# Kernel tuning notes

Hardware: AMD Instinct MI355X
Metric: run time of the kernel (lower is better)

Reference implementation:

```python
import jax, jax.numpy as jnp
import numpy as np


def setup_inputs() -> dict:
    key = jax.random.key(0)
    k1, k2, k3 = jax.random.split(key, 3)
    B, K, OUT, IN = 8192, 8, 1024, 1024
    bound = (6.0 / (IN * OUT)) ** 0.5
    x = jax.random.normal(k1, (B, IN), dtype=jnp.float32)
    expert_weights = jax.random.uniform(k2, (B, K), dtype=jnp.float32)
    weight = jax.random.uniform(k3, (K, OUT, IN), dtype=jnp.float32, minval=-bound, maxval=bound)
    bias = jnp.zeros((K, OUT), dtype=jnp.float32)
    return {"x": x, "expert_weights": expert_weights, "weight": weight, "bias": bias}


def reference(x, expert_weights, weight, bias):
    # Mathematically identical to: blended_W = einsum('bk,koi->boi'); bmm(blended_W, x)
    # but avoids materializing the [B,out,in] intermediate: apply each expert's
    # linear map then blend with routing weights (contraction reassociation).
    per_expert = jnp.einsum('bi,koi->bko', x, weight)        # [B, K, out]
    y = jnp.einsum('bk,bko->bo', expert_weights, per_expert)  # [B, out]
    y = y + expert_weights @ bias                             # blended bias [B, out]
    return y
```

## Files before the change

### kernel.cpp

```cpp
#include <hip/hip_runtime.h>
#include <hip/hip_bf16.h>

typedef __attribute__((ext_vector_type(8))) short short8;
typedef __attribute__((ext_vector_type(4))) float f32x4;

#define NDIM 1024
#define INDIM 1024
#define KEXP 8
#define BROWS 8192
#define NX (BROWS * INDIM)
#define NW (KEXP * NDIM * INDIM)

#define BM 256
#define BN 128
#define BK 64
#define NT 128
#define ABUF 16384
#define BBUF 8192
#define BUFU (ABUF + BBUF)

__device__ __forceinline__ unsigned int pack2bf(float a, float b) {
    __hip_bfloat162 h = __float22bfloat162_rn(make_float2(a, b));
    union { __hip_bfloat162 h; unsigned int u; } cv;
    cv.h = h;
    return cv.u;
}

__device__ __forceinline__ void gload16(const void* src, void* ldsdst) {
    __builtin_amdgcn_global_load_lds(
        (__attribute__((address_space(1))) void*)(src),
        (__attribute__((address_space(3))) void*)(ldsdst), 16, 0, 0);
}

__global__ void convert_bf16(const float* __restrict__ x, const float* __restrict__ w,
                             unsigned short* __restrict__ dst) {
    const long total = (long)NX + NW;
    const long stride = (long)gridDim.x * blockDim.x * 8;
    for (long i = ((long)blockIdx.x * blockDim.x + threadIdx.x) * 8; i < total; i += stride) {
        const float* s = (i < NX) ? (x + i) : (w + (i - NX));
        float4 a = ((const float4*)s)[0];
        float4 b = ((const float4*)s)[1];
        uint4 q;
        q.x = pack2bf(a.x, a.y); q.y = pack2bf(a.z, a.w);
        q.z = pack2bf(b.x, b.y); q.w = pack2bf(b.z, b.w);
        *(uint4*)(dst + i) = q;
    }
}

__global__ __launch_bounds__(512, 2)
void moe_gemm_pipe(const unsigned short* __restrict__ ab,
                   const float* __restrict__ ew,
                   const float* __restrict__ bias,
                   float* __restrict__ out) {
    __shared__ __align__(16) unsigned short lds[3 * BUFU];

    const int tid = threadIdx.x;
    const int bid = blockIdx.x;
    const int nt = bid & 7;
    const int mt = bid >> 3;
    const int mbase = mt * BM;
    const int nbase = nt * BN;

    const int w  = tid >> 6;
    const int l  = tid & 63;
    const int lr = l & 15;
    const int lg = l >> 4;
    const int wrow = (w >> 1) * 64;
    const int wcol = (w & 1) * 64;

    const int lrow = l >> 2;
    const int sg = (l & 3) ^ ((l >> 3) & 3);

    const unsigned short* Xb = ab;
    const unsigned short* Wb = ab + NX;

    const int swz = (lr >> 1) & 3;
    int aoff[4][2], boff[4][2];
#pragma unroll
    for (int m = 0; m < 4; ++m)
#pragma unroll
        for (int ks = 0; ks < 2; ++ks)
            aoff[m][ks] = ks * 8192 + (wrow + m * 16 + lr) * 32 + ((lg ^ swz) * 8);
#pragma unroll
    for (int n = 0; n < 4; ++n)
#pragma unroll
        for (int ks = 0; ks < 2; ++ks)
            boff[n][ks] = ABUF + ks * 4096 + (wcol + n * 16 + lr) * 32 + ((lg ^ swz) * 8);

    auto stageA = [&](int buf, int kt, int i) {
        const int c = i * 8 + w;
        const int ks = c >> 4, rg = c & 15;
        const unsigned short* src = Xb + (size_t)(mbase + rg * 16 + lrow) * INDIM
                                  + (size_t)((kt & 15) * 64 + ks * 32 + sg * 8);
        gload16(src, &lds[buf * BUFU + c * 512]);
    };
    auto stageB = [&](int buf, int kt, int i) {
        const int c = i * 8 + w;
        const int ks = c >> 3, rg = c & 7;
        const unsigned short* src = Wb + (size_t)(kt >> 4) * (NDIM * INDIM)
                                  + (size_t)(nbase + rg * 16 + lrow) * INDIM
                                  + (size_t)((kt & 15) * 64 + ks * 32 + sg * 8);
        gload16(src, &lds[buf * BUFU + ABUF + c * 512]);
    };

    f32x4 acc[4][4], accT[4][4];
#pragma unroll
    for (int m = 0; m < 4; ++m)
#pragma unroll
        for (int n = 0; n < 4; ++n) {
            acc[m][n] = f32x4{0.f, 0.f, 0.f, 0.f};
            accT[m][n] = f32x4{0.f, 0.f, 0.f, 0.f};
        }

#pragma unroll
    for (int t = 0; t < 2; ++t) {
        stageA(t, t, 0); stageA(t, t, 1); stageA(t, t, 2); stageA(t, t, 3);
        stageB(t, t, 0); stageB(t, t, 1);
    }

    int bufR = 0, bufS = 2;
#pragma unroll 1
    for (int kt = 0; kt < NT; ++kt) {
        const bool doS = (kt + 2) < NT;
        const bool bnd = (kt & 15) == 15;

        if (kt < NT - 2)
            asm volatile("s_waitcnt vmcnt(6)\n\ts_barrier" ::: "memory");
        else
            asm volatile("s_waitcnt vmcnt(0)\n\ts_barrier" ::: "memory");

        float e0[4][4];
        if (bnd) {
            const int eidx = kt >> 4;
#pragma unroll
            for (int m = 0; m < 4; ++m)
#pragma unroll
                for (int j = 0; j < 4; ++j)
                    e0[m][j] = ew[(size_t)(mbase + wrow + m * 16 + lg * 4 + j) * KEXP + eidx];
        }

        const unsigned short* lb = &lds[bufR * BUFU];
        short8 a0[4], b0[4], a1[4], b1[4];

#pragma unroll
        for (int m = 0; m < 4; ++m) a0[m] = *(const short8*)(lb + aoff[m][0]);
#pragma unroll
        for (int n = 0; n < 4; ++n) b0[n] = *(const short8*)(lb + boff[n][0]);

        if (doS) {
            stageA(bufS, kt + 2, 0); stageA(bufS, kt + 2, 1);
            stageA(bufS, kt + 2, 2); stageA(bufS, kt + 2, 3);
            stageB(bufS, kt + 2, 0); stageB(bufS, kt + 2, 1);
        }

#pragma unroll
        for (int m = 0; m < 4; ++m) a1[m] = *(const short8*)(lb + aoff[m][1]);
#pragma unroll
        for (int n = 0; n < 4; ++n) b1[n] = *(const short8*)(lb + boff[n][1]);

        __builtin_amdgcn_s_setprio(1);
#pragma unroll
        for (int m = 0; m < 4; ++m)
#pragma unroll
            for (int n = 0; n < 4; ++n)
                acc[m][n] = __builtin_amdgcn_mfma_f32_16x16x32_bf16(a0[m], b0[n], acc[m][n], 0, 0, 0);
        __builtin_amdgcn_s_setprio(0);

        __builtin_amdgcn_s_setprio(1);
#pragma unroll
        for (int m = 0; m < 4; ++m)
#pragma unroll
            for (int n = 0; n < 4; ++n)
                acc[m][n] = __builtin_amdgcn_mfma_f32_16x16x32_bf16(a1[m], b1[n], acc[m][n], 0, 0, 0);
        __builtin_amdgcn_s_setprio(0);

        if (bnd) {
#pragma unroll
            for (int m = 0; m < 4; ++m)
#pragma unroll
                for (int n = 0; n < 4; ++n) {
#pragma unroll
                    for (int j = 0; j < 4; ++j)
                        accT[m][n][j] += e0[m][j] * acc[m][n][j];
                    acc[m][n] = f32x4{0.f, 0.f, 0.f, 0.f};
                }
        }

        bufR = (bufR == 2) ? 0 : bufR + 1;
        bufS = (bufS == 2) ? 0 : bufS + 1;
    }

    float bv[4][8];
#pragma unroll
    for (int n = 0; n < 4; ++n) {
        const int gc = nbase + wcol + n * 16 + lr;
#pragma unroll
        for (int kk = 0; kk < 8; ++kk) bv[n][kk] = bias[kk * NDIM + gc];
    }
#pragma unroll
    for (int m = 0; m < 4; ++m)
#pragma unroll
        for (int j = 0; j < 4; ++j) {
            const int grow = mbase + wrow + m * 16 + lg * 4 + j;
            const float4* e4 = (const float4*)(ew + (size_t)grow * KEXP);
            const float4 ea = e4[0];
            const float4 eb = e4[1];
            const float ev[8] = {ea.x, ea.y, ea.z, ea.w, eb.x, eb.y, eb.z, eb.w};
            float* op = out + (size_t)grow * NDIM + nbase + wcol;
#pragma unroll
            for (int n = 0; n < 4; ++n) {
                float t = accT[m][n][j];
#pragma unroll
                for (int kk = 0; kk < 8; ++kk) t += ev[kk] * bv[n][kk];
                op[n * 16 + lr] = t;
            }
        }
}

#define FLDW 40
__global__ __launch_bounds__(256, 2)
void moe_blend_gemm_fb(const float* __restrict__ x, const float* __restrict__ ew,
                       const float* __restrict__ w, const float* __restrict__ bias,
                       float* __restrict__ out) {
    __shared__ unsigned short lA[128][FLDW];
    __shared__ unsigned short lB[128][FLDW];
    const int tid = threadIdx.x, bid = blockIdx.x;
    const int nt = bid & 7, mt = bid >> 3;
    const int mbase = mt * 128, nbase = nt * 128;
    const int trow = tid >> 1, tcol = (tid & 1) * 16;
    const float* xp = x + (size_t)(mbase + trow) * INDIM + tcol;
    const float* wp = w + (size_t)(nbase + trow) * INDIM + tcol;
    const float* ep = ew + (size_t)(mbase + trow) * KEXP;
    const int wid = tid >> 6, wrB = (wid >> 1) * 64, wcB = (wid & 1) * 64;
    const int l = tid & 63, lr = l & 15, lg = l >> 4;
    f32x4 acc[4][4];
#pragma unroll
    for (int m = 0; m < 4; ++m)
#pragma unroll
        for (int n = 0; n < 4; ++n) acc[m][n] = f32x4{0.f, 0.f, 0.f, 0.f};
    const unsigned short* rdA = &lA[wrB + lr][lg * 8];
    const unsigned short* rdB = &lB[wcB + lr][lg * 8];
    unsigned int* wA = (unsigned int*)&lA[trow][tcol];
    unsigned int* wB = (unsigned int*)&lB[trow][tcol];
    float4 ra0, ra1, ra2, ra3, rb0, rb1, rb2, rb3;
    float sc;
    {
        const float4* pa = (const float4*)(xp);
        ra0 = pa[0]; ra1 = pa[1]; ra2 = pa[2]; ra3 = pa[3];
        const float4* pb = (const float4*)(wp);
        rb0 = pb[0]; rb1 = pb[1]; rb2 = pb[2]; rb3 = pb[3];
        sc = ep[0];
    }
    for (int tt = 0; tt < 256; ++tt) {
        __syncthreads();
        uint4 qa0, qa1, qb0, qb1;
        qa0.x = pack2bf(ra0.x * sc, ra0.y * sc); qa0.y = pack2bf(ra0.z * sc, ra0.w * sc);
        qa0.z = pack2bf(ra1.x * sc, ra1.y * sc); qa0.w = pack2bf(ra1.z * sc, ra1.w * sc);
        qa1.x = pack2bf(ra2.x * sc, ra2.y * sc); qa1.y = pack2bf(ra2.z * sc, ra2.w * sc);
        qa1.z = pack2bf(ra3.x * sc, ra3.y * sc); qa1.w = pack2bf(ra3.z * sc, ra3.w * sc);
        qb0.x = pack2bf(rb0.x, rb0.y); qb0.y = pack2bf(rb0.z, rb0.w);
        qb0.z = pack2bf(rb1.x, rb1.y); qb0.w = pack2bf(rb1.z, rb1.w);
        qb1.x = pack2bf(rb2.x, rb2.y); qb1.y = pack2bf(rb2.z, rb2.w);
        qb1.z = pack2bf(rb3.x, rb3.y); qb1.w = pack2bf(rb3.z, rb3.w);
        *(uint4*)(wA) = qa0; *(uint4*)(wA + 4) = qa1;
        *(uint4*)(wB) = qb0; *(uint4*)(wB + 4) = qb1;
        __syncthreads();
        if (tt + 1 < 256) {
            const int kc = (tt + 1) >> 5, i0 = ((tt + 1) & 31) * 32;
            const float4* pa = (const float4*)(xp + i0);
            ra0 = pa[0]; ra1 = pa[1]; ra2 = pa[2]; ra3 = pa[3];
            const float4* pb = (const float4*)(wp + (size_t)kc * (size_t)(NDIM * INDIM) + i0);
            rb0 = pb[0]; rb1 = pb[1]; rb2 = pb[2]; rb3 = pb[3];
            sc = ep[kc];
        }
        short8 af[4], bf[4];
#pragma unroll
        for (int m = 0; m < 4; ++m) af[m] = *(const short8*)(rdA + m * 16 * FLDW);
#pragma unroll
        for (int n = 0; n < 4; ++n) bf[n] = *(const short8*)(rdB + n * 16 * FLDW);
#pragma unroll
        for (int m = 0; m < 4; ++m)
#pragma unroll
            for (int n = 0; n < 4; ++n)
                acc[m][n] = __builtin_amdgcn_mfma_f32_16x16x32_bf16(af[m], bf[n], acc[m][n], 0, 0, 0);
    }
#pragma unroll
    for (int m = 0; m < 4; ++m)
#pragma unroll
        for (int j = 0; j < 4; ++j) {
            const int gr = mbase + wrB + m * 16 + lg * 4 + j;
            const float4* e4 = (const float4*)(ew + (size_t)gr * KEXP);
            const float4 e0 = e4[0], e1 = e4[1];
            const float eb[8] = {e0.x, e0.y, e0.z, e0.w, e1.x, e1.y, e1.z, e1.w};
            float* op = out + (size_t)gr * NDIM + nbase + wcB;
#pragma unroll
            for (int n = 0; n < 4; ++n) {
                float t = acc[m][n][j];
#pragma unroll
                for (int kk = 0; kk < 8; ++kk) t += eb[kk] * bias[kk * NDIM + nbase + wcB + n * 16 + lr];
                op[n * 16 + lr] = t;
            }
        }
}

extern "C" void kernel_launch(void* const* d_in, const int* in_sizes, int n_in,
                              void* d_out, int out_size, void* d_ws, size_t ws_size,
                              hipStream_t stream) {
    (void)in_sizes; (void)n_in; (void)out_size;
    const float* x    = (const float*)d_in[0];
    const float* ew   = (const float*)d_in[1];
    const float* w    = (const float*)d_in[2];
    const float* bias = (const float*)d_in[3];
    float* out = (float*)d_out;

    const size_t need = (size_t)(NX + NW) * sizeof(unsigned short);
    if (ws_size >= need) {
        unsigned short* ab = (unsigned short*)d_ws;
        hipLaunchKernelGGL(convert_bf16, dim3(2048), dim3(256), 0, stream, x, w, ab);
        hipLaunchKernelGGL(moe_gemm_pipe, dim3(256), dim3(512), 0, stream, ab, ew, bias, out);
    } else {
        hipLaunchKernelGGL(moe_blend_gemm_fb, dim3(512), dim3(256), 0, stream, x, ew, w, bias, out);
    }
}
```

Before: 180.1 us.

## Fold routing weights into expanded A and split-K GEMM with bf16 partials

Adds a new path that builds a pre-scaled activation matrix A'[b, k*IN+i] = ew[b,k]*x[b,i] in bf16, so the whole op becomes a single GEMM over K*IN. The GEMM uses 256x256 tiles and a two-way split along the reduction, writing bf16 partials that a separate reduce kernel sums and then adds the blended bias to. This removes the per-k-tile accumulator rescaling and the ew loads from the inner loop. In exchange it materialises a 128 MB A' buffer, rounds partials to bf16, and adds extra launches. The old fallback kernel is removed, so no path runs when the workspace is too small.

New measurement: 167.8 us. 1.07x faster.

```diff
diff --git a/kernel.cpp b/kernel.cpp
--- a/kernel.cpp
+++ b/kernel.cpp
@@ -10,6 +10,227 @@
 #define BROWS 8192
 #define NX (BROWS * INDIM)
 #define NW (KEXP * NDIM * INDIM)
+#define NA (BROWS * KEXP * INDIM)
+#define NPH (BROWS * NDIM)
+
+__device__ __forceinline__ unsigned int pack2bf(float a, float b) {
+    __hip_bfloat162 h = __float22bfloat162_rn(make_float2(a, b));
+    union { __hip_bfloat162 h; unsigned int u; } cv;
+    cv.h = h;
+    return cv.u;
+}
+
+__device__ __forceinline__ float bf2f(unsigned short u) {
+    return __uint_as_float(((unsigned int)u) << 16);
+}
+
+__device__ __forceinline__ void gload16(const void* src, void* ldsdst) {
+    __builtin_amdgcn_global_load_lds(
+        (__attribute__((address_space(1))) void*)(src),
+        (__attribute__((address_space(3))) void*)(ldsdst), 16, 0, 0);
+}
+
+
+__global__ void convert_a(const float* __restrict__ x, const float* __restrict__ ew,
+                          unsigned short* __restrict__ Ap) {
+    const int t = blockIdx.x * blockDim.x + threadIdx.x;
+    if (t >= (BROWS * INDIM / 8)) return;
+    const int b = t >> 7;
+    const int i0 = (t & 127) * 8;
+    const float4 xa = *(const float4*)(x + (size_t)b * INDIM + i0);
+    const float4 xb = *(const float4*)(x + (size_t)b * INDIM + i0 + 4);
+    const float4 ea = *(const float4*)(ew + (size_t)b * KEXP);
+    const float4 e2 = *(const float4*)(ew + (size_t)b * KEXP + 4);
+    const float e[8] = {ea.x, ea.y, ea.z, ea.w, e2.x, e2.y, e2.z, e2.w};
+    unsigned short* dst = Ap + (size_t)b * (KEXP * INDIM) + i0;
+#pragma unroll
+    for (int k = 0; k < 8; ++k) {
+        const float s = e[k];
+        uint4 q;
+        q.x = pack2bf(xa.x * s, xa.y * s);
+        q.y = pack2bf(xa.z * s, xa.w * s);
+        q.z = pack2bf(xb.x * s, xb.y * s);
+        q.w = pack2bf(xb.z * s, xb.w * s);
+        *(uint4*)(dst + (size_t)k * INDIM) = q;
+    }
+}
+
+__global__ void convert_w(const float* __restrict__ w, unsigned short* __restrict__ Wp) {
+    const long i = ((long)blockIdx.x * blockDim.x + threadIdx.x) * 8;
+    if (i >= NW) return;
+    const float4 a = ((const float4*)(w + i))[0];
+    const float4 b = ((const float4*)(w + i))[1];
+    uint4 q;
+    q.x = pack2bf(a.x, a.y); q.y = pack2bf(a.z, a.w);
+    q.z = pack2bf(b.x, b.y); q.w = pack2bf(b.z, b.w);
+    *(uint4*)(Wp + i) = q;
+}
+
+__global__ __launch_bounds__(512, 2)
+void moe_gemm_ks(const unsigned short* __restrict__ Ap,
+                 const unsigned short* __restrict__ Wp,
+                 unsigned short* __restrict__ Pp) {
+    __shared__ __align__(16) unsigned short lds[2 * 32768];
+
+    const int tid = threadIdx.x;
+    const int bid = blockIdx.x;
+    const int comp = bid & 7;
+    const int nt = comp >> 1;
+    const int h  = comp & 1;
+    const int mt = bid >> 3;
+    const int mbase = mt * 256;
+    const int nbase = nt * 256;
+    const int kofs = h * 4096;
+
+    const int w  = tid >> 6;
+    const int l  = tid & 63;
+    const int lr = l & 15;
+    const int lg = l >> 4;
+    const int wrow = (w >> 2) * 128;
+    const int wcol = (w & 3) * 64;
+
+    const int lrow = l >> 2;
+    const int sg = (l & 3) ^ ((l >> 3) & 3);
+    const int swz = (lr >> 1) & 3;
+
+    int aoff[8][2], boff[4][2];
+#pragma unroll
+    for (int mf = 0; mf < 8; ++mf)
+#pragma unroll
+        for (int ks = 0; ks < 2; ++ks)
+            aoff[mf][ks] = ks * 8192 + (wrow + mf * 16 + lr) * 32 + ((lg ^ swz) * 8);
+#pragma unroll
+    for (int nf = 0; nf < 4; ++nf)
+#pragma unroll
+        for (int ks = 0; ks < 2; ++ks)
+            boff[nf][ks] = 16384 + ks * 8192 + (wcol + nf * 16 + lr) * 32 + ((lg ^ swz) * 8);
+
+    auto stage4 = [&](int slot, int kt, int half) {
+#pragma unroll
+        for (int i = 0; i < 4; ++i) {
+            const int id = w * 8 + half * 4 + i;
+            unsigned short* dst = &lds[slot * 32768 + id * 512];
+            const int ks = (id >> 4) & 1;
+            const int sub = id & 15;
+            const int kcb = kofs + kt * 64 + ks * 32 + sg * 8;
+            if (id < 32) {
+                gload16(Ap + (size_t)(mbase + sub * 16 + lrow) * (KEXP * INDIM) + kcb, dst);
+            } else {
+                gload16(Wp + (size_t)(kcb >> 10) * (NDIM * INDIM)
+                           + (size_t)(nbase + sub * 16 + lrow) * INDIM + (kcb & 1023), dst);
+            }
+        }
+    };
+
+    f32x4 acc[8][4];
+#pragma unroll
+    for (int mf = 0; mf < 8; ++mf)
+#pragma unroll
+        for (int nf = 0; nf < 4; ++nf) acc[mf][nf] = f32x4{0.f, 0.f, 0.f, 0.f};
+
+    stage4(0, 0, 0);
+    stage4(0, 0, 1);
+
+#pragma unroll 1
+    for (int kt = 0; kt < 64; ++kt) {
+        const int cs = kt & 1;
+        const bool doS = (kt + 1) < 64;
+
+        asm volatile("s_waitcnt vmcnt(0)\n\ts_barrier" ::: "memory");
+
+        const unsigned short* lb = &lds[cs * 32768];
+        short8 alo[4], ahi[4], b0[4], b1[4];
+
+#pragma unroll
+        for (int m = 0; m < 4; ++m) alo[m] = *(const short8*)(lb + aoff[m][0]);
+#pragma unroll
+        for (int n = 0; n < 4; ++n) b0[n] = *(const short8*)(lb + boff[n][0]);
+        if (doS) stage4(cs ^ 1, kt + 1, 0);
+#pragma unroll
+        for (int m = 0; m < 4; ++m) ahi[m] = *(const short8*)(lb + aoff[4 + m][0]);
+
+        __builtin_amdgcn_s_setprio(1);
+#pragma unroll
+        for (int m = 0; m < 4; ++m)
+#pragma unroll
+            for (int n = 0; n < 4; ++n)
+                acc[m][n] = __builtin_amdgcn_mfma_f32_16x16x32_bf16(alo[m], b0[n], acc[m][n], 0, 0, 0);
+        __builtin_amdgcn_s_setprio(0);
+
+#pragma unroll
+        for (int n = 0; n < 4; ++n) b1[n] = *(const short8*)(lb + boff[n][1]);
+#pragma unroll
+        for (int m = 0; m < 4; ++m) alo[m] = *(const short8*)(lb + aoff[m][1]);
+        if (doS) stage4(cs ^ 1, kt + 1, 1);
+
+        __builtin_amdgcn_s_setprio(1);
+#pragma unroll
+        for (int m = 0; m < 4; ++m)
+#pragma unroll
+            for (int n = 0; n < 4; ++n)
+                acc[4 + m][n] = __builtin_amdgcn_mfma_f32_16x16x32_bf16(ahi[m], b0[n], acc[4 + m][n], 0, 0, 0);
+        __builtin_amdgcn_s_setprio(0);
+
+#pragma unroll
+        for (int m = 0; m < 4; ++m) ahi[m] = *(const short8*)(lb + aoff[4 + m][1]);
+
+        __builtin_amdgcn_s_setprio(1);
+#pragma unroll
+        for (int m = 0; m < 4; ++m)
+#pragma unroll
+            for (int n = 0; n < 4; ++n)
+                acc[m][n] = __builtin_amdgcn_mfma_f32_16x16x32_bf16(alo[m], b1[n], acc[m][n], 0, 0, 0);
+        __builtin_amdgcn_s_setprio(0);
+
+        __builtin_amdgcn_s_setprio(1);
+#pragma unroll
+        for (int m = 0; m < 4; ++m)
+#pragma unroll
+            for (int n = 0; n < 4; ++n)
+                acc[4 + m][n] = __builtin_amdgcn_mfma_f32_16x16x32_bf16(ahi[m], b1[n], acc[4 + m][n], 0, 0, 0);
+        __builtin_amdgcn_s_setprio(0);
+    }
+
+#pragma unroll
+    for (int mf = 0; mf < 8; ++mf)
+#pragma unroll
+        for (int j = 0; j < 4; ++j) {
+            const int grow = mbase + wrow + mf * 16 + lg * 4 + j;
+            unsigned short* op = Pp + (size_t)h * NPH + (size_t)grow * NDIM + nbase + wcol;
+#pragma unroll
+            for (int nf = 0; nf < 4; ++nf) {
+                union { __hip_bfloat16 hh; unsigned short u; } cv;
+                cv.hh = __float2bfloat16(acc[mf][nf][j]);
+                op[nf * 16 + lr] = cv.u;
+            }
+        }
+}
+
+__global__ void reduce_blend(const unsigned short* __restrict__ Pp,
+                             const float* __restrict__ ew,
+                             const float* __restrict__ bias,
+                             float* __restrict__ out) {
+    const long base = ((long)blockIdx.x * blockDim.x + threadIdx.x) * 8;
+    if (base >= NPH) return;
+    const int b = (int)(base >> 10);
+    const int o = (int)(base & 1023);
+    const short8 p0 = *(const short8*)(Pp + base);
+    const short8 p1 = *(const short8*)(Pp + NPH + base);
+    const float4 ea = *(const float4*)(ew + (size_t)b * KEXP);
+    const float4 e2 = *(const float4*)(ew + (size_t)b * KEXP + 4);
+    const float e[8] = {ea.x, ea.y, ea.z, ea.w, e2.x, e2.y, e2.z, e2.w};
+    float r[8];
+#pragma unroll
+    for (int j = 0; j < 8; ++j)
+        r[j] = bf2f((unsigned short)p0[j]) + bf2f((unsigned short)p1[j]);
+#pragma unroll
+    for (int k = 0; k < 8; ++k)
+#pragma unroll
+        for (int j = 0; j < 8; ++j) r[j] += e[k] * bias[k * NDIM + o + j];
+    *(float4*)(out + base) = make_float4(r[0], r[1], r[2], r[3]);
+    *(float4*)(out + base + 4) = make_float4(r[4], r[5], r[6], r[7]);
+}
+
 
 #define BM 256
 #define BN 128
@@ -18,19 +239,6 @@
 #define ABUF 16384
 #define BBUF 8192
 #define BUFU (ABUF + BBUF)
-
-__device__ __forceinline__ unsigned int pack2bf(float a, float b) {
-    __hip_bfloat162 h = __float22bfloat162_rn(make_float2(a, b));
-    union { __hip_bfloat162 h; unsigned int u; } cv;
-    cv.h = h;
-    return cv.u;
-}
-
-__device__ __forceinline__ void gload16(const void* src, void* ldsdst) {
-    __builtin_amdgcn_global_load_lds(
-        (__attribute__((address_space(1))) void*)(src),
-        (__attribute__((address_space(3))) void*)(ldsdst), 16, 0, 0);
-}
 
 __global__ void convert_bf16(const float* __restrict__ x, const float* __restrict__ w,
                              unsigned short* __restrict__ dst) {
@@ -141,18 +349,15 @@
 
         const unsigned short* lb = &lds[bufR * BUFU];
         short8 a0[4], b0[4], a1[4], b1[4];
-
 #pragma unroll
         for (int m = 0; m < 4; ++m) a0[m] = *(const short8*)(lb + aoff[m][0]);
 #pragma unroll
         for (int n = 0; n < 4; ++n) b0[n] = *(const short8*)(lb + boff[n][0]);
-
         if (doS) {
             stageA(bufS, kt + 2, 0); stageA(bufS, kt + 2, 1);
             stageA(bufS, kt + 2, 2); stageA(bufS, kt + 2, 3);
             stageB(bufS, kt + 2, 0); stageB(bufS, kt + 2, 1);
         }
-
 #pragma unroll
         for (int m = 0; m < 4; ++m) a1[m] = *(const short8*)(lb + aoff[m][1]);
 #pragma unroll
@@ -165,7 +370,6 @@
             for (int n = 0; n < 4; ++n)
                 acc[m][n] = __builtin_amdgcn_mfma_f32_16x16x32_bf16(a0[m], b0[n], acc[m][n], 0, 0, 0);
         __builtin_amdgcn_s_setprio(0);
-
         __builtin_amdgcn_s_setprio(1);
 #pragma unroll
         for (int m = 0; m < 4; ++m)
@@ -212,92 +416,6 @@
                 float t = accT[m][n][j];
 #pragma unroll
                 for (int kk = 0; kk < 8; ++kk) t += ev[kk] * bv[n][kk];
-                op[n * 16 + lr] = t;
-            }
-        }
-}
-
-#define FLDW 40
-__global__ __launch_bounds__(256, 2)
-void moe_blend_gemm_fb(const float* __restrict__ x, const float* __restrict__ ew,
-                       const float* __restrict__ w, const float* __restrict__ bias,
-                       float* __restrict__ out) {
-    __shared__ unsigned short lA[128][FLDW];
-    __shared__ unsigned short lB[128][FLDW];
-    const int tid = threadIdx.x, bid = blockIdx.x;
-    const int nt = bid & 7, mt = bid >> 3;
-    const int mbase = mt * 128, nbase = nt * 128;
-    const int trow = tid >> 1, tcol = (tid & 1) * 16;
-    const float* xp = x + (size_t)(mbase + trow) * INDIM + tcol;
-    const float* wp = w + (size_t)(nbase + trow) * INDIM + tcol;
-    const float* ep = ew + (size_t)(mbase + trow) * KEXP;
-    const int wid = tid >> 6, wrB = (wid >> 1) * 64, wcB = (wid & 1) * 64;
-    const int l = tid & 63, lr = l & 15, lg = l >> 4;
-    f32x4 acc[4][4];
-#pragma unroll
-    for (int m = 0; m < 4; ++m)
-#pragma unroll
-        for (int n = 0; n < 4; ++n) acc[m][n] = f32x4{0.f, 0.f, 0.f, 0.f};
-    const unsigned short* rdA = &lA[wrB + lr][lg * 8];
-    const unsigned short* rdB = &lB[wcB + lr][lg * 8];
-    unsigned int* wA = (unsigned int*)&lA[trow][tcol];
-    unsigned int* wB = (unsigned int*)&lB[trow][tcol];
-    float4 ra0, ra1, ra2, ra3, rb0, rb1, rb2, rb3;
-    float sc;
-    {
-        const float4* pa = (const float4*)(xp);
-        ra0 = pa[0]; ra1 = pa[1]; ra2 = pa[2]; ra3 = pa[3];
-        const float4* pb = (const float4*)(wp);
-        rb0 = pb[0]; rb1 = pb[1]; rb2 = pb[2]; rb3 = pb[3];
-        sc = ep[0];
-    }
-    for (int tt = 0; tt < 256; ++tt) {
-        __syncthreads();
-        uint4 qa0, qa1, qb0, qb1;
-        qa0.x = pack2bf(ra0.x * sc, ra0.y * sc); qa0.y = pack2bf(ra0.z * sc, ra0.w * sc);
-        qa0.z = pack2bf(ra1.x * sc, ra1.y * sc); qa0.w = pack2bf(ra1.z * sc, ra1.w * sc);
-        qa1.x = pack2bf(ra2.x * sc, ra2.y * sc); qa1.y = pack2bf(ra2.z * sc, ra2.w * sc);
-        qa1.z = pack2bf(ra3.x * sc, ra3.y * sc); qa1.w = pack2bf(ra3.z * sc, ra3.w * sc);
-        qb0.x = pack2bf(rb0.x, rb0.y); qb0.y = pack2bf(rb0.z, rb0.w);
-        qb0.z = pack2bf(rb1.x, rb1.y); qb0.w = pack2bf(rb1.z, rb1.w);
-        qb1.x = pack2bf(rb2.x, rb2.y); qb1.y = pack2bf(rb2.z, rb2.w);
-        qb1.z = pack2bf(rb3.x, rb3.y); qb1.w = pack2bf(rb3.z, rb3.w);
-        *(uint4*)(wA) = qa0; *(uint4*)(wA + 4) = qa1;
-        *(uint4*)(wB) = qb0; *(uint4*)(wB + 4) = qb1;
-        __syncthreads();
-        if (tt + 1 < 256) {
-            const int kc = (tt + 1) >> 5, i0 = ((tt + 1) & 31) * 32;
-            const float4* pa = (const float4*)(xp + i0);
-            ra0 = pa[0]; ra1 = pa[1]; ra2 = pa[2]; ra3 = pa[3];
-            const float4* pb = (const float4*)(wp + (size_t)kc * (size_t)(NDIM * INDIM) + i0);
-            rb0 = pb[0]; rb1 = pb[1]; rb2 = pb[2]; rb3 = pb[3];
-            sc = ep[kc];
-        }
-        short8 af[4], bf[4];
-#pragma unroll
-        for (int m = 0; m < 4; ++m) af[m] = *(const short8*)(rdA + m * 16 * FLDW);
-#pragma unroll
-        for (int n = 0; n < 4; ++n) bf[n] = *(const short8*)(rdB + n * 16 * FLDW);
-#pragma unroll
-        for (int m = 0; m < 4; ++m)
-#pragma unroll
-            for (int n = 0; n < 4; ++n)
-                acc[m][n] = __builtin_amdgcn_mfma_f32_16x16x32_bf16(af[m], bf[n], acc[m][n], 0, 0, 0);
-    }
-#pragma unroll
-    for (int m = 0; m < 4; ++m)
-#pragma unroll
-        for (int j = 0; j < 4; ++j) {
-            const int gr = mbase + wrB + m * 16 + lg * 4 + j;
-            const float4* e4 = (const float4*)(ew + (size_t)gr * KEXP);
-            const float4 e0 = e4[0], e1 = e4[1];
-            const float eb[8] = {e0.x, e0.y, e0.z, e0.w, e1.x, e1.y, e1.z, e1.w};
-            float* op = out + (size_t)gr * NDIM + nbase + wcB;
-#pragma unroll
-            for (int n = 0; n < 4; ++n) {
-                float t = acc[m][n][j];
-#pragma unroll
-                for (int kk = 0; kk < 8; ++kk) t += eb[kk] * bias[kk * NDIM + nbase + wcB + n * 16 + lr];
                 op[n * 16 + lr] = t;
             }
         }
@@ -313,12 +431,20 @@
     const float* bias = (const float*)d_in[3];
     float* out = (float*)d_out;
 
-    const size_t need = (size_t)(NX + NW) * sizeof(unsigned short);
-    if (ws_size >= need) {
+    const size_t needA = ((size_t)NA + NW + 2 * (size_t)NPH) * sizeof(unsigned short);
+    const size_t needB = (size_t)(NX + NW) * sizeof(unsigned short);
+
+    if (ws_size >= needA) {
+        unsigned short* Ap = (unsigned short*)d_ws;
+        unsigned short* Wp = Ap + NA;
+        unsigned short* Pp = Wp + NW;
+        hipLaunchKernelGGL(convert_a, dim3(4096), dim3(256), 0, stream, x, ew, Ap);
+        hipLaunchKernelGGL(convert_w, dim3(4096), dim3(256), 0, stream, w, Wp);
+        hipLaunchKernelGGL(moe_gemm_ks, dim3(256), dim3(512), 0, stream, Ap, Wp, Pp);
+        hipLaunchKernelGGL(reduce_blend, dim3(4096), dim3(256), 0, stream, Pp, ew, bias, out);
+    } else if (ws_size >= needB) {
         unsigned short* ab = (unsigned short*)d_ws;
         hipLaunchKernelGGL(convert_bf16, dim3(2048), dim3(256), 0, stream, x, w, ab);
         hipLaunchKernelGGL(moe_gemm_pipe, dim3(256), dim3(512), 0, stream, ab, ew, bias, out);
-    } else {
-        hipLaunchKernelGGL(moe_blend_gemm_fb, dim3(512), dim3(256), 0, stream, x, ew, w, bias, out);
-    }
-}
+    }
+}
```

## Fold experts into GEMM N dimension and blend in epilogue via LDS

Applied to the files above, without the earlier changes.

Restructures the GEMM so each block computes a 256-row by 32-output tile across all 8 experts at once, treating the K*OUT dimension as N. The reduction shrinks to the 1024-wide input, and the expert blend moves to the epilogue, where shuffles and an LDS buffer replace the per-expert accumulate step. The grid becomes 1024 blocks with an XCD-aware tile mapping, and the pipeline changes from triple to double buffering with a full vmcnt(0) wait each step. The conversion kernel grid is also doubled. In exchange, the x tile is reused across eight experts, but the full wait before each barrier may expose load latency.

Measured after the change: 145.9 us (median of 3 runs). -19.0%, faster.

```diff
diff --git a/kernel.cpp b/kernel.cpp
--- a/kernel.cpp
+++ b/kernel.cpp
@@ -10,14 +10,6 @@
 #define BROWS 8192
 #define NX (BROWS * INDIM)
 #define NW (KEXP * NDIM * INDIM)
-
-#define BM 256
-#define BN 128
-#define BK 64
-#define NT 128
-#define ABUF 16384
-#define BBUF 8192
-#define BUFU (ABUF + BBUF)
 
 __device__ __forceinline__ unsigned int pack2bf(float a, float b) {
     __hip_bfloat162 h = __float22bfloat162_rn(make_float2(a, b));
@@ -48,173 +40,175 @@
 }
 
 __global__ __launch_bounds__(512, 2)
-void moe_gemm_pipe(const unsigned short* __restrict__ ab,
+void moe_gemm_fold(const unsigned short* __restrict__ xb,
                    const float* __restrict__ ew,
+                   const unsigned short* __restrict__ Wp,
                    const float* __restrict__ bias,
                    float* __restrict__ out) {
-    __shared__ __align__(16) unsigned short lds[3 * BUFU];
+    __shared__ __align__(16) unsigned short lds[2 * 32768];
 
     const int tid = threadIdx.x;
     const int bid = blockIdx.x;
-    const int nt = bid & 7;
-    const int mt = bid >> 3;
-    const int mbase = mt * BM;
-    const int nbase = nt * BN;
+    const int xcd = bid & 7;
+    const int grp = bid >> 3;
+    const int bt = xcd * 4 + (grp & 3);
+    const int ot = grp >> 2;
+    const int bbase = bt * 256;
+    const int o_blk = ot * 32;
 
     const int w  = tid >> 6;
     const int l  = tid & 63;
     const int lr = l & 15;
     const int lg = l >> 4;
-    const int wrow = (w >> 1) * 64;
-    const int wcol = (w & 1) * 64;
+    const int wrow = (w >> 2) * 128;
+    const int wcol = (w & 3) * 64;
 
     const int lrow = l >> 2;
     const int sg = (l & 3) ^ ((l >> 3) & 3);
-
-    const unsigned short* Xb = ab;
-    const unsigned short* Wb = ab + NX;
-
     const int swz = (lr >> 1) & 3;
-    int aoff[4][2], boff[4][2];
-#pragma unroll
-    for (int m = 0; m < 4; ++m)
+
+    int aoff[8][2], boff[4][2];
+#pragma unroll
+    for (int mf = 0; mf < 8; ++mf)
 #pragma unroll
         for (int ks = 0; ks < 2; ++ks)
-            aoff[m][ks] = ks * 8192 + (wrow + m * 16 + lr) * 32 + ((lg ^ swz) * 8);
-#pragma unroll
-    for (int n = 0; n < 4; ++n)
+            aoff[mf][ks] = ks * 8192 + (wrow + mf * 16 + lr) * 32 + ((lg ^ swz) * 8);
+#pragma unroll
+    for (int nf = 0; nf < 4; ++nf)
 #pragma unroll
         for (int ks = 0; ks < 2; ++ks)
-            boff[n][ks] = ABUF + ks * 4096 + (wcol + n * 16 + lr) * 32 + ((lg ^ swz) * 8);
-
-    auto stageA = [&](int buf, int kt, int i) {
-        const int c = i * 8 + w;
-        const int ks = c >> 4, rg = c & 15;
-        const unsigned short* src = Xb + (size_t)(mbase + rg * 16 + lrow) * INDIM
-                                  + (size_t)((kt & 15) * 64 + ks * 32 + sg * 8);
-        gload16(src, &lds[buf * BUFU + c * 512]);
+            boff[nf][ks] = 16384 + ks * 8192 + (wcol + nf * 16 + lr) * 32 + ((lg ^ swz) * 8);
+
+    auto stage4 = [&](int slot, int kt, int half) {
+#pragma unroll
+        for (int i = 0; i < 4; ++i) {
+            const int id = w * 8 + half * 4 + i;
+            unsigned short* dst = &lds[slot * 32768 + id * 512];
+            const int sub = id & 15;
+            const int col = kt * 64 + ((id >> 4) & 1) * 32 + sg * 8;
+            if (id < 32) {
+                gload16(Wp + (size_t)(lrow & 7) * (NDIM * INDIM)
+                           + (size_t)(o_blk + sub * 2 + (lrow >> 3)) * INDIM + col, dst);
+            } else {
+                gload16(xb + (size_t)(bbase + sub * 16 + lrow) * INDIM + col, dst);
+            }
+        }
     };
-    auto stageB = [&](int buf, int kt, int i) {
-        const int c = i * 8 + w;
-        const int ks = c >> 3, rg = c & 7;
-        const unsigned short* src = Wb + (size_t)(kt >> 4) * (NDIM * INDIM)
-                                  + (size_t)(nbase + rg * 16 + lrow) * INDIM
-                                  + (size_t)((kt & 15) * 64 + ks * 32 + sg * 8);
-        gload16(src, &lds[buf * BUFU + ABUF + c * 512]);
-    };
-
-    f32x4 acc[4][4], accT[4][4];
-#pragma unroll
-    for (int m = 0; m < 4; ++m)
-#pragma unroll
-        for (int n = 0; n < 4; ++n) {
-            acc[m][n] = f32x4{0.f, 0.f, 0.f, 0.f};
-            accT[m][n] = f32x4{0.f, 0.f, 0.f, 0.f};
-        }
-
-#pragma unroll
-    for (int t = 0; t < 2; ++t) {
-        stageA(t, t, 0); stageA(t, t, 1); stageA(t, t, 2); stageA(t, t, 3);
-        stageB(t, t, 0); stageB(t, t, 1);
-    }
-
-    int bufR = 0, bufS = 2;
+
+    f32x4 acc[8][4];
+#pragma unroll
+    for (int mf = 0; mf < 8; ++mf)
+#pragma unroll
+        for (int nf = 0; nf < 4; ++nf) acc[mf][nf] = f32x4{0.f, 0.f, 0.f, 0.f};
+
+    stage4(0, 0, 0);
+    stage4(0, 0, 1);
+
 #pragma unroll 1
-    for (int kt = 0; kt < NT; ++kt) {
-        const bool doS = (kt + 2) < NT;
-        const bool bnd = (kt & 15) == 15;
-
-        if (kt < NT - 2)
-            asm volatile("s_waitcnt vmcnt(6)\n\ts_barrier" ::: "memory");
-        else
-            asm volatile("s_waitcnt vmcnt(0)\n\ts_barrier" ::: "memory");
-
-        float e0[4][4];
-        if (bnd) {
-            const int eidx = kt >> 4;
-#pragma unroll
-            for (int m = 0; m < 4; ++m)
-#pragma unroll
-                for (int j = 0; j < 4; ++j)
-                    e0[m][j] = ew[(size_t)(mbase + wrow + m * 16 + lg * 4 + j) * KEXP + eidx];
-        }
-
-        const unsigned short* lb = &lds[bufR * BUFU];
-        short8 a0[4], b0[4], a1[4], b1[4];
-
-#pragma unroll
-        for (int m = 0; m < 4; ++m) a0[m] = *(const short8*)(lb + aoff[m][0]);
+    for (int kt = 0; kt < 16; ++kt) {
+        const int cs = kt & 1;
+        const bool doS = (kt + 1) < 16;
+
+        asm volatile("s_waitcnt vmcnt(0)\n\ts_barrier" ::: "memory");
+
+        const unsigned short* lb = &lds[cs * 32768];
+        short8 alo[4], ahi[4], b0[4], b1[4];
+
+#pragma unroll
+        for (int m = 0; m < 4; ++m) alo[m] = *(const short8*)(lb + aoff[m][0]);
 #pragma unroll
         for (int n = 0; n < 4; ++n) b0[n] = *(const short8*)(lb + boff[n][0]);
-
-        if (doS) {
-            stageA(bufS, kt + 2, 0); stageA(bufS, kt + 2, 1);
-            stageA(bufS, kt + 2, 2); stageA(bufS, kt + 2, 3);
-            stageB(bufS, kt + 2, 0); stageB(bufS, kt + 2, 1);
-        }
-
-#pragma unroll
-        for (int m = 0; m < 4; ++m) a1[m] = *(const short8*)(lb + aoff[m][1]);
+        if (doS) stage4(cs ^ 1, kt + 1, 0);
+#pragma unroll
+        for (int m = 0; m < 4; ++m) ahi[m] = *(const short8*)(lb + aoff[4 + m][0]);
+
+        __builtin_amdgcn_s_setprio(1);
+#pragma unroll
+        for (int m = 0; m < 4; ++m)
+#pragma unroll
+            for (int n = 0; n < 4; ++n)
+                acc[m][n] = __builtin_amdgcn_mfma_f32_16x16x32_bf16(alo[m], b0[n], acc[m][n], 0, 0, 0);
+        __builtin_amdgcn_s_setprio(0);
+
 #pragma unroll
         for (int n = 0; n < 4; ++n) b1[n] = *(const short8*)(lb + boff[n][1]);
+#pragma unroll
+        for (int m = 0; m < 4; ++m) alo[m] = *(const short8*)(lb + aoff[m][1]);
+        if (doS) stage4(cs ^ 1, kt + 1, 1);
 
         __builtin_amdgcn_s_setprio(1);
 #pragma unroll
         for (int m = 0; m < 4; ++m)
 #pragma unroll
             for (int n = 0; n < 4; ++n)
-                acc[m][n] = __builtin_amdgcn_mfma_f32_16x16x32_bf16(a0[m], b0[n], acc[m][n], 0, 0, 0);
+                acc[4 + m][n] = __builtin_amdgcn_mfma_f32_16x16x32_bf16(ahi[m], b0[n], acc[4 + m][n], 0, 0, 0);
         __builtin_amdgcn_s_setprio(0);
 
+#pragma unroll
+        for (int m = 0; m < 4; ++m) ahi[m] = *(const short8*)(lb + aoff[4 + m][1]);
+
         __builtin_amdgcn_s_setprio(1);
 #pragma unroll
         for (int m = 0; m < 4; ++m)
 #pragma unroll
             for (int n = 0; n < 4; ++n)
-                acc[m][n] = __builtin_amdgcn_mfma_f32_16x16x32_bf16(a1[m], b1[n], acc[m][n], 0, 0, 0);
+                acc[m][n] = __builtin_amdgcn_mfma_f32_16x16x32_bf16(alo[m], b1[n], acc[m][n], 0, 0, 0);
         __builtin_amdgcn_s_setprio(0);
 
-        if (bnd) {
-#pragma unroll
-            for (int m = 0; m < 4; ++m)
-#pragma unroll
-                for (int n = 0; n < 4; ++n) {
-#pragma unroll
-                    for (int j = 0; j < 4; ++j)
-                        accT[m][n][j] += e0[m][j] * acc[m][n][j];
-                    acc[m][n] = f32x4{0.f, 0.f, 0.f, 0.f};
-                }
-        }
-
-        bufR = (bufR == 2) ? 0 : bufR + 1;
-        bufS = (bufS == 2) ? 0 : bufS + 1;
-    }
-
-    float bv[4][8];
-#pragma unroll
-    for (int n = 0; n < 4; ++n) {
-        const int gc = nbase + wcol + n * 16 + lr;
-#pragma unroll
-        for (int kk = 0; kk < 8; ++kk) bv[n][kk] = bias[kk * NDIM + gc];
-    }
-#pragma unroll
-    for (int m = 0; m < 4; ++m)
-#pragma unroll
-        for (int j = 0; j < 4; ++j) {
-            const int grow = mbase + wrow + m * 16 + lg * 4 + j;
-            const float4* e4 = (const float4*)(ew + (size_t)grow * KEXP);
-            const float4 ea = e4[0];
-            const float4 eb = e4[1];
-            const float ev[8] = {ea.x, ea.y, ea.z, ea.w, eb.x, eb.y, eb.z, eb.w};
-            float* op = out + (size_t)grow * NDIM + nbase + wcol;
-#pragma unroll
-            for (int n = 0; n < 4; ++n) {
-                float t = accT[m][n][j];
-#pragma unroll
-                for (int kk = 0; kk < 8; ++kk) t += ev[kk] * bv[n][kk];
-                op[n * 16 + lr] = t;
-            }
-        }
+        __builtin_amdgcn_s_setprio(1);
+#pragma unroll
+        for (int m = 0; m < 4; ++m)
+#pragma unroll
+            for (int n = 0; n < 4; ++n)
+                acc[4 + m][n] = __builtin_amdgcn_mfma_f32_16x16x32_bf16(ahi[m], b1[n], acc[4 + m][n], 0, 0, 0);
+        __builtin_amdgcn_s_setprio(0);
+    }
+
+    __syncthreads();
+    float* ylds = (float*)lds;
+
+    const int obw = wrow >> 3;
+#pragma unroll
+    for (int nf = 0; nf < 4; ++nf) {
+        const int bl = wcol + nf * 16 + lr;
+        const float4 ea = *(const float4*)(ew + (size_t)(bbase + bl) * KEXP);
+        const float4 eb = *(const float4*)(ew + (size_t)(bbase + bl) * KEXP + 4);
+        float c0, c1, c2, c3;
+        if (lg & 1) { c0 = eb.x; c1 = eb.y; c2 = eb.z; c3 = eb.w; }
+        else        { c0 = ea.x; c1 = ea.y; c2 = ea.z; c3 = ea.w; }
+#pragma unroll
+        for (int mf = 0; mf < 8; ++mf) {
+            float p = c0 * acc[mf][nf][0] + c1 * acc[mf][nf][1]
+                    + c2 * acc[mf][nf][2] + c3 * acc[mf][nf][3];
+            p += __shfl_xor(p, 16);
+            if (!(lg & 1))
+                ylds[bl * 36 + obw + mf * 2 + (lg >> 1)] = p;
+        }
+    }
+    __syncthreads();
+
+    {
+        const int b = tid >> 1;
+        const int oh = (tid & 1) * 16;
+        const float* yr = &ylds[b * 36 + oh];
+        float y0[16];
+#pragma unroll
+        for (int jj = 0; jj < 16; ++jj) y0[jj] = yr[jj];
+        const float4 ea = *(const float4*)(ew + (size_t)(bbase + b) * KEXP);
+        const float4 e2 = *(const float4*)(ew + (size_t)(bbase + b) * KEXP + 4);
+        const float ekk[8] = {ea.x, ea.y, ea.z, ea.w, e2.x, e2.y, e2.z, e2.w};
+#pragma unroll
+        for (int k = 0; k < 8; ++k) {
+            const float* bp = bias + k * NDIM + o_blk + oh;
+#pragma unroll
+            for (int jj = 0; jj < 16; ++jj) y0[jj] += ekk[k] * bp[jj];
+        }
+        float* op = out + (size_t)(bbase + b) * NDIM + o_blk + oh;
+#pragma unroll
+        for (int jj = 0; jj < 4; ++jj)
+            *(float4*)(op + jj * 4) =
+                make_float4(y0[jj * 4], y0[jj * 4 + 1], y0[jj * 4 + 2], y0[jj * 4 + 3]);
+    }
 }
 
 #define FLDW 40
@@ -314,10 +308,12 @@
     float* out = (float*)d_out;
 
     const size_t need = (size_t)(NX + NW) * sizeof(unsigned short);
+
     if (ws_size >= need) {
-        unsigned short* ab = (unsigned short*)d_ws;
-        hipLaunchKernelGGL(convert_bf16, dim3(2048), dim3(256), 0, stream, x, w, ab);
-        hipLaunchKernelGGL(moe_gemm_pipe, dim3(256), dim3(512), 0, stream, ab, ew, bias, out);
+        unsigned short* xb = (unsigned short*)d_ws;
+        unsigned short* Wp = xb + NX;
+        hipLaunchKernelGGL(convert_bf16, dim3(4096), dim3(256), 0, stream, x, w, xb);
+        hipLaunchKernelGGL(moe_gemm_fold, dim3(1024), dim3(512), 0, stream, xb, ew, Wp, bias, out);
     } else {
         hipLaunchKernelGGL(moe_blend_gemm_fb, dim3(512), dim3(256), 0, stream, x, ew, w, bias, out);
     }
```
